# Kernel optimization log

Hardware: AMD Instinct MI355X
Metric: run time of the kernel (lower is better)

The kernel has to match this reference:

```python
import jax, jax.numpy as jnp
import numpy as np

B = 8192          # num_envs
OPT = 16          # num options
SHARED = 22       # shared_state_size (hardcoded in module)
UNIQ = 8          # unique_state_size (hardcoded in module)
MIN_DUR, MAX_DUR = 0.1, 0.5  # const.gait_net.valid_swing_duration_range


def _w(k, o, i):
    return jax.random.normal(k, (o, i), jnp.float32) * (1.0 / np.sqrt(i))


def setup_inputs() -> dict:
    key = jax.random.key(0)
    ks = jax.random.split(key, 20)
    obs = jax.random.normal(ks[0], (B, SHARED + OPT * UNIQ), jnp.float32)
    flag = jax.random.uniform(ks[1], (B, OPT)) < 0.25
    u = obs[:, SHARED:].reshape(B, OPT, UNIQ)
    u = u.at[:, :, 0].set(jnp.where(flag, 1.0, u[:, :, 0]))
    obs = jnp.concatenate([obs[:, :SHARED], u.reshape(B, OPT * UNIQ)], axis=1)
    return {
        "obs": obs,
        "sw1": _w(ks[2], 256, 22), "sb1": jnp.zeros((256,), jnp.float32),
        "sw2": _w(ks[3], 256, 256), "sb2": jnp.zeros((256,), jnp.float32),
        "uw1": _w(ks[4], 128, 8), "ub1": jnp.zeros((128,), jnp.float32),
        "uw2": _w(ks[5], 128, 128), "ub2": jnp.zeros((128,), jnp.float32),
        "no_op_embedding": jax.random.normal(ks[6], (128,), jnp.float32),
        "tw1": _w(ks[7], 512, 384), "tb1": jnp.zeros((512,), jnp.float32),
        "tw2": _w(ks[8], 256, 512), "tb2": jnp.zeros((256,), jnp.float32),
        "vw": _w(ks[9], 1, 256), "vb": jnp.zeros((1,), jnp.float32),
        "dw": _w(ks[10], 1, 256), "db": jnp.zeros((1,), jnp.float32),
    }


def reference(obs, sw1, sb1, sw2, sb2, uw1, ub1, uw2, ub2, no_op_embedding,
              tw1, tb1, tw2, tb2, vw, vb, dw, db):
    relu = jax.nn.relu
    shared = obs[:, :SHARED]                               # [B, 22]
    uniq = obs[:, SHARED:].reshape(B, OPT, UNIQ)           # [B, OPT, 8]
    # shared encoder (22 -> 256 -> 256, relu output)
    se = relu(relu(shared @ sw1.T + sb1) @ sw2.T + sb2)    # [B, 256]
    # unique encoder applied to all options at once (8 -> 128 -> 128)
    ue = relu(relu(uniq @ uw1.T + ub1) @ uw2.T + ub2)      # [B, OPT, 128]
    no_op = uniq[:, :, 0] == 1.0                           # [B, OPT]
    ue = jnp.where(no_op[..., None], no_op_embedding, ue)
    trunk_in = jnp.concatenate(
        [jnp.broadcast_to(se[:, None, :], (B, OPT, se.shape[-1])), ue], axis=-1)
    t = relu(relu(trunk_in @ tw1.T + tb1) @ tw2.T + tb2)   # [B, OPT, 256]
    logits = (t @ vw.T + vb).squeeze(-1)                   # [B, OPT]
    duration = jax.nn.sigmoid((t @ dw.T + db).squeeze(-1)) * (MAX_DUR - MIN_DUR) + MIN_DUR
    return logits, duration
```

## Files before the change

kernel.cpp:

```cpp
#include <hip/hip_runtime.h>
#include <stdint.h>


static constexpr int B_ = 8192;

typedef __attribute__((ext_vector_type(8))) short bf16x8;
typedef __attribute__((ext_vector_type(4))) float f32x4;

__device__ __forceinline__ float u2f(uint16_t u) {
    union { uint32_t i; float f; } c; c.i = (uint32_t)u << 16; return c.f;
}
__device__ __forceinline__ uint16_t f2u(float f) {
    union { float f; uint32_t i; } c; c.f = f;
    uint32_t x = c.i;
    return (uint16_t)((x + 0x7FFFu + ((x >> 16) & 1u)) >> 16);
}
__device__ __forceinline__ bf16x8 cvt8(float4 a, float4 b) {
    bf16x8 r;
    r[0] = (short)f2u(a.x); r[1] = (short)f2u(a.y);
    r[2] = (short)f2u(a.z); r[3] = (short)f2u(a.w);
    r[4] = (short)f2u(b.x); r[5] = (short)f2u(b.y);
    r[6] = (short)f2u(b.z); r[7] = (short)f2u(b.w);
    return r;
}

static constexpr size_t WCSE   = 0;
static constexpr size_t WTW1UE = 4194304;
static constexpr size_t WTW2   = WTW1UE + 65536;
static constexpr size_t WUW2   = WTW2 + 131072;

__global__ __launch_bounds__(256) void k_front(
    const float* __restrict__ obs,
    const float* __restrict__ sw1, const float* __restrict__ sb1,
    const float* __restrict__ sw2f, const float* __restrict__ sb2,
    const float* __restrict__ tw1, const float* __restrict__ tb1,
    const float* __restrict__ tw2, const float* __restrict__ uw2,
    uint16_t* __restrict__ ws)
{
    __shared__ float xs[32][24];
    __shared__ uint16_t h1sf[32 * 264];
    __shared__ uint16_t seL[32 * 264];
    const int t = threadIdx.x;

    if (t < 208) {
        int g4 = blockIdx.x * 208 + t;
        const float* src; size_t dst;
        if (g4 < 16384) {
            int n = g4 >> 5, w = g4 & 31;
            src = tw1 + (size_t)(n * 96 + 64 + w) * 4;
            dst = WTW1UE + (size_t)(n * 32 + w) * 4;
        } else if (g4 < 49152) {
            int q = g4 - 16384;
            src = tw2 + (size_t)q * 4; dst = WTW2 + (size_t)q * 4;
        } else {
            int q = g4 - 49152;
            src = uw2 + (size_t)q * 4; dst = WUW2 + (size_t)q * 4;
        }
        float4 v = *reinterpret_cast<const float4*>(src);
        ushort4 o;
        o.x = f2u(v.x); o.y = f2u(v.y); o.z = f2u(v.z); o.w = f2u(v.w);
        *reinterpret_cast<ushort4*>(ws + dst) = o;
    }

    const int b0 = blockIdx.x * 32;
    for (int i = t; i < 704; i += 256) {
        int e = i / 22, c = i - e * 22;
        xs[e][c] = obs[(size_t)(b0 + e) * 150 + c];
    }
    __syncthreads();
    {
        float w[22];
        #pragma unroll
        for (int k = 0; k < 22; ++k) w[k] = sw1[t * 22 + k];
        const float bias = sb1[t];
        #pragma unroll
        for (int e = 0; e < 32; ++e) {
            float a = bias;
            #pragma unroll
            for (int k = 0; k < 22; ++k) a += w[k] * xs[e][k];
            h1sf[e * 264 + t] = f2u(fmaxf(a, 0.f));
        }
    }
    __syncthreads();
    const int wv = t >> 6, lane = t & 63, quad = lane >> 4, l16 = lane & 15;
    {
        f32x4 acc[2][4];
        #pragma unroll
        for (int nt = 0; nt < 4; ++nt) {
            float bv = sb2[wv * 64 + nt * 16 + l16];
            acc[0][nt] = {bv, bv, bv, bv};
            acc[1][nt] = {bv, bv, bv, bv};
        }
        #pragma unroll
        for (int kk = 0; kk < 8; ++kk) {
            bf16x8 af[2];
            #pragma unroll
            for (int mt = 0; mt < 2; ++mt)
                af[mt] = *reinterpret_cast<const bf16x8*>(
                    &h1sf[(mt * 16 + l16) * 264 + kk * 32 + quad * 8]);
            #pragma unroll
            for (int nt = 0; nt < 4; ++nt) {
                const float* wr = sw2f + (size_t)(wv * 64 + nt * 16 + l16) * 256
                                  + kk * 32 + quad * 8;
                bf16x8 bf = cvt8(*reinterpret_cast<const float4*>(wr),
                                 *reinterpret_cast<const float4*>(wr + 4));
                #pragma unroll
                for (int mt = 0; mt < 2; ++mt)
                    acc[mt][nt] = __builtin_amdgcn_mfma_f32_16x16x32_bf16(
                        af[mt], bf, acc[mt][nt], 0, 0, 0);
            }
        }
        #pragma unroll
        for (int mt = 0; mt < 2; ++mt)
            #pragma unroll
            for (int nt = 0; nt < 4; ++nt)
                #pragma unroll
                for (int r = 0; r < 4; ++r)
                    seL[(mt * 16 + quad * 4 + r) * 264 + wv * 64 + nt * 16 + l16] =
                        f2u(fmaxf(acc[mt][nt][r], 0.f));
    }
    __syncthreads();
    {
        f32x4 acc[2][8];
        #pragma unroll
        for (int nt = 0; nt < 8; ++nt) {
            float bv = tb1[wv * 128 + nt * 16 + l16];
            acc[0][nt] = {bv, bv, bv, bv};
            acc[1][nt] = {bv, bv, bv, bv};
        }
        #pragma unroll
        for (int kk = 0; kk < 8; ++kk) {
            bf16x8 af[2];
            #pragma unroll
            for (int mt = 0; mt < 2; ++mt)
                af[mt] = *reinterpret_cast<const bf16x8*>(
                    &seL[(mt * 16 + l16) * 264 + kk * 32 + quad * 8]);
            #pragma unroll
            for (int nt = 0; nt < 8; ++nt) {
                const float* wr = tw1 + (size_t)(wv * 128 + nt * 16 + l16) * 384
                                  + kk * 32 + quad * 8;
                bf16x8 bf = cvt8(*reinterpret_cast<const float4*>(wr),
                                 *reinterpret_cast<const float4*>(wr + 4));
                #pragma unroll
                for (int mt = 0; mt < 2; ++mt)
                    acc[mt][nt] = __builtin_amdgcn_mfma_f32_16x16x32_bf16(
                        af[mt], bf, acc[mt][nt], 0, 0, 0);
            }
        }
        #pragma unroll
        for (int mt = 0; mt < 2; ++mt)
            #pragma unroll
            for (int nt = 0; nt < 8; ++nt)
                #pragma unroll
                for (int r = 0; r < 4; ++r)
                    ws[WCSE + (size_t)(b0 + mt * 16 + quad * 4 + r) * 512 +
                       wv * 128 + nt * 16 + l16] = f2u(acc[mt][nt][r]);
    }
}

static constexpr int UQ_OFF   = 0;
static constexpr int NOOP_OFF = 2112;
static constexpr int CSE_OFF  = 2368;
static constexpr int H1U_OFF  = 6464;
static constexpr int UET_OFF  = 23872;
static constexpr int H1T_OFF  = 41280;
static constexpr int SMEM_SZ  = 75072;

__global__ __launch_bounds__(512, 4) void k_main(
    const float* __restrict__ obs,
    const float* __restrict__ uw1, const float* __restrict__ ub1,
    const float* __restrict__ ub2, const float* __restrict__ emb,
    const float* __restrict__ tb2,
    const float* __restrict__ vw,  const float* __restrict__ vb,
    const float* __restrict__ dw,  const float* __restrict__ db,
    const uint16_t* __restrict__ wsb,
    float* __restrict__ out)
{
    __shared__ __align__(16) char smem[SMEM_SZ];
    float*    uq    = (float*)(smem + UQ_OFF);
    float*    noopf = (float*)(smem + NOOP_OFF);
    uint16_t* cseL  = (uint16_t*)(smem + CSE_OFF);
    uint16_t* h1u   = (uint16_t*)(smem + H1U_OFF);
    uint16_t* uet   = (uint16_t*)(smem + UET_OFF);
    uint16_t* h1t   = (uint16_t*)(smem + H1T_OFF);
    uint16_t* t2    = h1t;

    const int t    = threadIdx.x;
    const int wv   = t >> 6;
    const int lane = t & 63;
    const int quad = lane >> 4;
    const int l16  = lane & 15;
    const int b0   = blockIdx.x * 4;

    const uint16_t* csep  = wsb + WCSE;
    const uint16_t* tw1ue = wsb + WTW1UE;
    const uint16_t* tw2b  = wsb + WTW2;
    const uint16_t* uw2b  = wsb + WUW2;

    {
        int e = t >> 7, c = t & 127;
        uq[e * 132 + c] = obs[(size_t)(b0 + e) * 150 + 22 + c];
        #pragma unroll
        for (int ii = 0; ii < 2; ++ii) {
            int i = t + ii * 512;
            int ee = i >> 8, cc = i & 255;
            ((uint32_t*)cseL)[ee * 256 + cc] =
                ((const uint32_t*)(csep + (size_t)(b0 + ee) * 512))[cc];
        }
        if (t < 64) {
            int ee = t >> 4, o = t & 15;
            noopf[t] = (obs[(size_t)(b0 + ee) * 150 + 22 + o * 8] == 1.0f) ? 1.0f : 0.0f;
        }
    }
    __syncthreads();

    {
        const int n = t & 127, h = t >> 7;
        float w[8];
        #pragma unroll
        for (int k = 0; k < 8; ++k) w[k] = uw1[n * 8 + k];
        const float bias = ub1[n];
        #pragma unroll
        for (int ii = 0; ii < 16; ++ii) {
            int row = h * 16 + ii;
            const float4* xp = (const float4*)&uq[h * 132 + ii * 8];
            float4 xa = xp[0], xb = xp[1];
            float a = bias + w[0] * xa.x + w[1] * xa.y + w[2] * xa.z + w[3] * xa.w
                           + w[4] * xb.x + w[5] * xb.y + w[6] * xb.z + w[7] * xb.w;
            h1u[row * 136 + n] = f2u(fmaxf(a, 0.f));
        }
    }
    __syncthreads();

    {
        const int n = wv * 16 + l16;
        const float bv = ub2[n];
        const float ev = emb[n];
        f32x4 acc[4];
        #pragma unroll
        for (int mt = 0; mt < 4; ++mt) acc[mt] = {bv, bv, bv, bv};
        #pragma unroll
        for (int kk = 0; kk < 4; ++kk) {
            bf16x8 bf = *reinterpret_cast<const bf16x8*>(
                &uw2b[(size_t)n * 128 + kk * 32 + quad * 8]);
            #pragma unroll
            for (int mt = 0; mt < 4; ++mt) {
                bf16x8 af = *reinterpret_cast<const bf16x8*>(
                    &h1u[(mt * 16 + l16) * 136 + kk * 32 + quad * 8]);
                acc[mt] = __builtin_amdgcn_mfma_f32_16x16x32_bf16(af, bf, acc[mt], 0, 0, 0);
            }
        }
        #pragma unroll
        for (int mt = 0; mt < 4; ++mt)
            #pragma unroll
            for (int r = 0; r < 4; ++r) {
                int row = mt * 16 + quad * 4 + r;
                float v = (noopf[row] != 0.0f) ? ev : fmaxf(acc[mt][r], 0.f);
                uet[row * 136 + n] = f2u(v);
            }
    }
    __syncthreads();

    f32x4 acc2[4][2];
    #pragma unroll
    for (int nt = 0; nt < 2; ++nt) {
        float bv = tb2[wv * 32 + nt * 16 + l16];
        #pragma unroll
        for (int mt = 0; mt < 4; ++mt) acc2[mt][nt] = {bv, bv, bv, bv};
    }

    #pragma unroll
    for (int nc = 0; nc < 2; ++nc) {
        {
            f32x4 acc1[4][2];
            #pragma unroll
            for (int nt = 0; nt < 2; ++nt) {
                int n = nc * 256 + wv * 32 + nt * 16 + l16;
                #pragma unroll
                for (int mt = 0; mt < 4; ++mt) {
                    float v = u2f(cseL[mt * 512 + n]);
                    acc1[mt][nt] = {v, v, v, v};
                }
            }
            const uint16_t* bb = tw1ue + (size_t)(nc * 256 + wv * 32 + l16) * 128
                                 + quad * 8;
            bf16x8 bc[2], bn[2];
            bc[0] = *reinterpret_cast<const bf16x8*>(bb);
            bc[1] = *reinterpret_cast<const bf16x8*>(bb + 2048);
            #pragma unroll
            for (int kk = 0; kk < 4; ++kk) {
                if (kk < 3) {
                    bn[0] = *reinterpret_cast<const bf16x8*>(bb + (kk + 1) * 32);
                    bn[1] = *reinterpret_cast<const bf16x8*>(bb + 2048 + (kk + 1) * 32);
                }
                bf16x8 af[4];
                #pragma unroll
                for (int mt = 0; mt < 4; ++mt)
                    af[mt] = *reinterpret_cast<const bf16x8*>(
                        &uet[(mt * 16 + l16) * 136 + kk * 32 + quad * 8]);
                #pragma unroll
                for (int mt = 0; mt < 4; ++mt)
                    #pragma unroll
                    for (int nt = 0; nt < 2; ++nt)
                        acc1[mt][nt] = __builtin_amdgcn_mfma_f32_16x16x32_bf16(
                            af[mt], bc[nt], acc1[mt][nt], 0, 0, 0);
                bc[0] = bn[0]; bc[1] = bn[1];
            }
            #pragma unroll
            for (int mt = 0; mt < 4; ++mt)
                #pragma unroll
                for (int nt = 0; nt < 2; ++nt)
                    #pragma unroll
                    for (int r = 0; r < 4; ++r) {
                        int row = mt * 16 + quad * 4 + r;
                        h1t[row * 264 + wv * 32 + nt * 16 + l16] =
                            f2u(fmaxf(acc1[mt][nt][r], 0.f));
                    }
        }
        __syncthreads();
        {
            const uint16_t* cb = tw2b + (size_t)(wv * 32 + l16) * 512 + nc * 256
                                 + quad * 8;
            bf16x8 cc[2], cn[2];
            cc[0] = *reinterpret_cast<const bf16x8*>(cb);
            cc[1] = *reinterpret_cast<const bf16x8*>(cb + 8192);
            #pragma unroll
            for (int k2 = 0; k2 < 8; ++k2) {
                if (k2 < 7) {
                    cn[0] = *reinterpret_cast<const bf16x8*>(cb + (k2 + 1) * 32);
                    cn[1] = *reinterpret_cast<const bf16x8*>(cb + 8192 + (k2 + 1) * 32);
                }
                bf16x8 af[4];
                #pragma unroll
                for (int mt = 0; mt < 4; ++mt)
                    af[mt] = *reinterpret_cast<const bf16x8*>(
                        &h1t[(mt * 16 + l16) * 264 + k2 * 32 + quad * 8]);
                #pragma unroll
                for (int mt = 0; mt < 4; ++mt)
                    #pragma unroll
                    for (int nt = 0; nt < 2; ++nt)
                        acc2[mt][nt] = __builtin_amdgcn_mfma_f32_16x16x32_bf16(
                            af[mt], cc[nt], acc2[mt][nt], 0, 0, 0);
                cc[0] = cn[0]; cc[1] = cn[1];
            }
        }
        if (nc == 0) __syncthreads();
    }
    __syncthreads();
    #pragma unroll
    for (int mt = 0; mt < 4; ++mt)
        #pragma unroll
        for (int nt = 0; nt < 2; ++nt)
            #pragma unroll
            for (int r = 0; r < 4; ++r) {
                int row = mt * 16 + quad * 4 + r;
                t2[row * 264 + wv * 32 + nt * 16 + l16] =
                    f2u(fmaxf(acc2[mt][nt][r], 0.f));
            }
    __syncthreads();

    {
        float vwf[4], dwf[4];
        #pragma unroll
        for (int j = 0; j < 4; ++j) {
            vwf[j] = vw[lane + 64 * j];
            dwf[j] = dw[lane + 64 * j];
        }
        const float vbf = vb[0], dbf = db[0];
        #pragma unroll
        for (int rr = 0; rr < 8; ++rr) {
            int row = wv * 8 + rr;
            float sv = 0.f, sd = 0.f;
            #pragma unroll
            for (int j = 0; j < 4; ++j) {
                float tv = u2f(t2[row * 264 + lane + 64 * j]);
                sv += tv * vwf[j];
                sd += tv * dwf[j];
            }
            #pragma unroll
            for (int off = 32; off > 0; off >>= 1) {
                sv += __shfl_down(sv, off);
                sd += __shfl_down(sd, off);
            }
            if (lane == 0) {
                int g = blockIdx.x * 64 + row;
                out[g] = sv + vbf;
                float z = sd + dbf;
                float sig = 1.f / (1.f + __expf(-z));
                out[B_ * 16 + g] = sig * 0.4f + 0.1f;
            }
        }
    }
}

extern "C" void kernel_launch(void* const* d_in, const int* in_sizes, int n_in,
                              void* d_out, int out_size, void* d_ws, size_t ws_size,
                              hipStream_t stream) {
    const float* obs = (const float*)d_in[0];
    const float* sw1 = (const float*)d_in[1];
    const float* sb1 = (const float*)d_in[2];
    const float* sw2 = (const float*)d_in[3];
    const float* sb2 = (const float*)d_in[4];
    const float* uw1 = (const float*)d_in[5];
    const float* ub1 = (const float*)d_in[6];
    const float* uw2 = (const float*)d_in[7];
    const float* ub2 = (const float*)d_in[8];
    const float* emb = (const float*)d_in[9];
    const float* tw1 = (const float*)d_in[10];
    const float* tb1 = (const float*)d_in[11];
    const float* tw2 = (const float*)d_in[12];
    const float* tb2 = (const float*)d_in[13];
    const float* vw  = (const float*)d_in[14];
    const float* vb  = (const float*)d_in[15];
    const float* dw  = (const float*)d_in[16];
    const float* db  = (const float*)d_in[17];

    uint16_t* wsb = (uint16_t*)d_ws;

    k_front<<<256, 256, 0, stream>>>(obs, sw1, sb1, sw2, sb2,
                                     tw1, tb1, tw2, uw2, wsb);
    k_main<<<B_ / 4, 512, 0, stream>>>(obs, uw1, ub1, ub2, emb, tb2,
                                       vw, vb, dw, db, wsb, (float*)d_out);
}
```

Baseline: 258.7 us.

## Split weight conversion into separate kernel and prefetch bf16 weights in shared encoder

Weight fp32→bf16 conversion, now including sw2 and the shared-encoder part of tw1, moves into a dedicated k_conv kernel. The encoder kernel then reads pre-converted bf16 weights with a one-step register prefetch across the K loop. The encoder also processes 16 rows per block across 512 blocks instead of 32 rows across 256, which raises parallelism. The cost is an extra kernel launch, and each block now reloads the weights for fewer rows.

```diff
diff --git a/kernel.cpp b/kernel.cpp
--- a/kernel.cpp
+++ b/kernel.cpp
@@ -15,55 +15,60 @@
     uint32_t x = c.i;
     return (uint16_t)((x + 0x7FFFu + ((x >> 16) & 1u)) >> 16);
 }
-__device__ __forceinline__ bf16x8 cvt8(float4 a, float4 b) {
-    bf16x8 r;
-    r[0] = (short)f2u(a.x); r[1] = (short)f2u(a.y);
-    r[2] = (short)f2u(a.z); r[3] = (short)f2u(a.w);
-    r[4] = (short)f2u(b.x); r[5] = (short)f2u(b.y);
-    r[6] = (short)f2u(b.z); r[7] = (short)f2u(b.w);
-    return r;
-}
 
 static constexpr size_t WCSE   = 0;
-static constexpr size_t WTW1UE = 4194304;
+static constexpr size_t WTW1SE = 4194304;
+static constexpr size_t WTW1UE = WTW1SE + 131072;
 static constexpr size_t WTW2   = WTW1UE + 65536;
 static constexpr size_t WUW2   = WTW2 + 131072;
-
-__global__ __launch_bounds__(256) void k_front(
+static constexpr size_t WSW2   = WUW2 + 16384;
+
+__global__ __launch_bounds__(256) void k_conv(
+    const float* __restrict__ tw1, const float* __restrict__ tw2,
+    const float* __restrict__ uw2, const float* __restrict__ sw2,
+    uint16_t* __restrict__ ws)
+{
+    int i4 = blockIdx.x * 256 + threadIdx.x;
+    const float* src; size_t dst;
+    if (i4 < 32768) {
+        int g = i4 * 4, n = g >> 8, k = g & 255;
+        src = tw1 + (size_t)n * 384 + k;
+        dst = WTW1SE + (size_t)g;
+    } else if (i4 < 49152) {
+        int q = i4 - 32768, n = q >> 5, w = q & 31;
+        src = tw1 + (size_t)n * 384 + 256 + w * 4;
+        dst = WTW1UE + (size_t)n * 128 + w * 4;
+    } else if (i4 < 81920) {
+        int q = (i4 - 49152) * 4;
+        src = tw2 + q; dst = WTW2 + q;
+    } else if (i4 < 86016) {
+        int q = (i4 - 81920) * 4;
+        src = uw2 + q; dst = WUW2 + q;
+    } else {
+        int q = (i4 - 86016) * 4;
+        src = sw2 + q; dst = WSW2 + q;
+    }
+    float4 v = *reinterpret_cast<const float4*>(src);
+    ushort4 o;
+    o.x = f2u(v.x); o.y = f2u(v.y); o.z = f2u(v.z); o.w = f2u(v.w);
+    *reinterpret_cast<ushort4*>(ws + dst) = o;
+}
+
+__global__ __launch_bounds__(256) void k_cse(
     const float* __restrict__ obs,
     const float* __restrict__ sw1, const float* __restrict__ sb1,
-    const float* __restrict__ sw2f, const float* __restrict__ sb2,
-    const float* __restrict__ tw1, const float* __restrict__ tb1,
-    const float* __restrict__ tw2, const float* __restrict__ uw2,
+    const float* __restrict__ sb2, const float* __restrict__ tb1,
     uint16_t* __restrict__ ws)
 {
-    __shared__ float xs[32][24];
-    __shared__ uint16_t h1sf[32 * 264];
-    __shared__ uint16_t seL[32 * 264];
+    __shared__ float xs[16][24];
+    __shared__ uint16_t h1s[16 * 264];
+    __shared__ uint16_t seL[16 * 264];
     const int t = threadIdx.x;
-
-    if (t < 208) {
-        int g4 = blockIdx.x * 208 + t;
-        const float* src; size_t dst;
-        if (g4 < 16384) {
-            int n = g4 >> 5, w = g4 & 31;
-            src = tw1 + (size_t)(n * 96 + 64 + w) * 4;
-            dst = WTW1UE + (size_t)(n * 32 + w) * 4;
-        } else if (g4 < 49152) {
-            int q = g4 - 16384;
-            src = tw2 + (size_t)q * 4; dst = WTW2 + (size_t)q * 4;
-        } else {
-            int q = g4 - 49152;
-            src = uw2 + (size_t)q * 4; dst = WUW2 + (size_t)q * 4;
-        }
-        float4 v = *reinterpret_cast<const float4*>(src);
-        ushort4 o;
-        o.x = f2u(v.x); o.y = f2u(v.y); o.z = f2u(v.z); o.w = f2u(v.w);
-        *reinterpret_cast<ushort4*>(ws + dst) = o;
-    }
-
-    const int b0 = blockIdx.x * 32;
-    for (int i = t; i < 704; i += 256) {
+    const int b0 = blockIdx.x * 16;
+    const uint16_t* sw2b   = ws + WSW2;
+    const uint16_t* tw1seb = ws + WTW1SE;
+
+    for (int i = t; i < 352; i += 256) {
         int e = i / 22, c = i - e * 22;
         xs[e][c] = obs[(size_t)(b0 + e) * 150 + c];
     }
@@ -74,87 +79,87 @@
         for (int k = 0; k < 22; ++k) w[k] = sw1[t * 22 + k];
         const float bias = sb1[t];
         #pragma unroll
-        for (int e = 0; e < 32; ++e) {
+        for (int e = 0; e < 16; ++e) {
             float a = bias;
             #pragma unroll
             for (int k = 0; k < 22; ++k) a += w[k] * xs[e][k];
-            h1sf[e * 264 + t] = f2u(fmaxf(a, 0.f));
+            h1s[e * 264 + t] = f2u(fmaxf(a, 0.f));
         }
     }
     __syncthreads();
     const int wv = t >> 6, lane = t & 63, quad = lane >> 4, l16 = lane & 15;
     {
-        f32x4 acc[2][4];
+        f32x4 acc[4];
         #pragma unroll
         for (int nt = 0; nt < 4; ++nt) {
             float bv = sb2[wv * 64 + nt * 16 + l16];
-            acc[0][nt] = {bv, bv, bv, bv};
-            acc[1][nt] = {bv, bv, bv, bv};
-        }
+            acc[nt] = {bv, bv, bv, bv};
+        }
+        const uint16_t* bb = sw2b + (size_t)(wv * 64 + l16) * 256 + quad * 8;
+        bf16x8 bc[4], bn[4];
+        #pragma unroll
+        for (int nt = 0; nt < 4; ++nt)
+            bc[nt] = *reinterpret_cast<const bf16x8*>(bb + nt * 4096);
         #pragma unroll
         for (int kk = 0; kk < 8; ++kk) {
-            bf16x8 af[2];
-            #pragma unroll
-            for (int mt = 0; mt < 2; ++mt)
-                af[mt] = *reinterpret_cast<const bf16x8*>(
-                    &h1sf[(mt * 16 + l16) * 264 + kk * 32 + quad * 8]);
-            #pragma unroll
-            for (int nt = 0; nt < 4; ++nt) {
-                const float* wr = sw2f + (size_t)(wv * 64 + nt * 16 + l16) * 256
-                                  + kk * 32 + quad * 8;
-                bf16x8 bf = cvt8(*reinterpret_cast<const float4*>(wr),
-                                 *reinterpret_cast<const float4*>(wr + 4));
-                #pragma unroll
-                for (int mt = 0; mt < 2; ++mt)
-                    acc[mt][nt] = __builtin_amdgcn_mfma_f32_16x16x32_bf16(
-                        af[mt], bf, acc[mt][nt], 0, 0, 0);
-            }
-        }
-        #pragma unroll
-        for (int mt = 0; mt < 2; ++mt)
+            if (kk < 7) {
+                #pragma unroll
+                for (int nt = 0; nt < 4; ++nt)
+                    bn[nt] = *reinterpret_cast<const bf16x8*>(
+                        bb + nt * 4096 + (kk + 1) * 32);
+            }
+            bf16x8 af = *reinterpret_cast<const bf16x8*>(
+                &h1s[l16 * 264 + kk * 32 + quad * 8]);
             #pragma unroll
             for (int nt = 0; nt < 4; ++nt)
-                #pragma unroll
-                for (int r = 0; r < 4; ++r)
-                    seL[(mt * 16 + quad * 4 + r) * 264 + wv * 64 + nt * 16 + l16] =
-                        f2u(fmaxf(acc[mt][nt][r], 0.f));
-    }
-    __syncthreads();
-    {
-        f32x4 acc[2][8];
+                acc[nt] = __builtin_amdgcn_mfma_f32_16x16x32_bf16(
+                    af, bc[nt], acc[nt], 0, 0, 0);
+            #pragma unroll
+            for (int nt = 0; nt < 4; ++nt) bc[nt] = bn[nt];
+        }
+        #pragma unroll
+        for (int nt = 0; nt < 4; ++nt)
+            #pragma unroll
+            for (int r = 0; r < 4; ++r)
+                seL[(quad * 4 + r) * 264 + wv * 64 + nt * 16 + l16] =
+                    f2u(fmaxf(acc[nt][r], 0.f));
+    }
+    __syncthreads();
+    {
+        f32x4 acc[8];
         #pragma unroll
         for (int nt = 0; nt < 8; ++nt) {
             float bv = tb1[wv * 128 + nt * 16 + l16];
-            acc[0][nt] = {bv, bv, bv, bv};
-            acc[1][nt] = {bv, bv, bv, bv};
-        }
+            acc[nt] = {bv, bv, bv, bv};
+        }
+        const uint16_t* bb = tw1seb + (size_t)(wv * 128 + l16) * 256 + quad * 8;
+        bf16x8 bc[8], bn[8];
+        #pragma unroll
+        for (int nt = 0; nt < 8; ++nt)
+            bc[nt] = *reinterpret_cast<const bf16x8*>(bb + nt * 4096);
         #pragma unroll
         for (int kk = 0; kk < 8; ++kk) {
-            bf16x8 af[2];
-            #pragma unroll
-            for (int mt = 0; mt < 2; ++mt)
-                af[mt] = *reinterpret_cast<const bf16x8*>(
-                    &seL[(mt * 16 + l16) * 264 + kk * 32 + quad * 8]);
-            #pragma unroll
-            for (int nt = 0; nt < 8; ++nt) {
-                const float* wr = tw1 + (size_t)(wv * 128 + nt * 16 + l16) * 384
-                                  + kk * 32 + quad * 8;
-                bf16x8 bf = cvt8(*reinterpret_cast<const float4*>(wr),
-                                 *reinterpret_cast<const float4*>(wr + 4));
-                #pragma unroll
-                for (int mt = 0; mt < 2; ++mt)
-                    acc[mt][nt] = __builtin_amdgcn_mfma_f32_16x16x32_bf16(
-                        af[mt], bf, acc[mt][nt], 0, 0, 0);
-            }
-        }
-        #pragma unroll
-        for (int mt = 0; mt < 2; ++mt)
+            if (kk < 7) {
+                #pragma unroll
+                for (int nt = 0; nt < 8; ++nt)
+                    bn[nt] = *reinterpret_cast<const bf16x8*>(
+                        bb + nt * 4096 + (kk + 1) * 32);
+            }
+            bf16x8 af = *reinterpret_cast<const bf16x8*>(
+                &seL[l16 * 264 + kk * 32 + quad * 8]);
             #pragma unroll
             for (int nt = 0; nt < 8; ++nt)
-                #pragma unroll
-                for (int r = 0; r < 4; ++r)
-                    ws[WCSE + (size_t)(b0 + mt * 16 + quad * 4 + r) * 512 +
-                       wv * 128 + nt * 16 + l16] = f2u(acc[mt][nt][r]);
+                acc[nt] = __builtin_amdgcn_mfma_f32_16x16x32_bf16(
+                    af, bc[nt], acc[nt], 0, 0, 0);
+            #pragma unroll
+            for (int nt = 0; nt < 8; ++nt) bc[nt] = bn[nt];
+        }
+        #pragma unroll
+        for (int nt = 0; nt < 8; ++nt)
+            #pragma unroll
+            for (int r = 0; r < 4; ++r)
+                ws[WCSE + (size_t)(b0 + quad * 4 + r) * 512 +
+                   wv * 128 + nt * 16 + l16] = f2u(acc[nt][r]);
     }
 }
 
@@ -417,8 +422,8 @@
 
     uint16_t* wsb = (uint16_t*)d_ws;
 
-    k_front<<<256, 256, 0, stream>>>(obs, sw1, sb1, sw2, sb2,
-                                     tw1, tb1, tw2, uw2, wsb);
+    k_conv<<<400, 256, 0, stream>>>(tw1, tw2, uw2, sw2, wsb);
+    k_cse<<<512, 256, 0, stream>>>(obs, sw1, sb1, sb2, tb1, wsb);
     k_main<<<B_ / 4, 512, 0, stream>>>(obs, uw1, ub1, ub2, emb, tb2,
                                        vw, vb, dw, db, wsb, (float*)d_out);
 }
```

Result: faster. 241.9 us (-6.5%).
